# Optimization experiments

Hardware: AMD Instinct MI355X
Metric: run time of the kernel (lower is better)

The kernel has to match this reference:

```python
import jax, jax.numpy as jnp
import numpy as np

N_ITEMS = 1_000_000
N_FACTORS = 64

def setup_inputs() -> dict:
    key = jax.random.key(0)
    emb_weight = jax.random.normal(key, (N_ITEMS, N_FACTORS), dtype=jnp.float32)
    return {"emb_weight": emb_weight, "item_idx": 12345, "size": 50}

def reference(emb_weight, item_idx, size):
    # gather query row: u = emb(ind)  -> [d]
    u = emb_weight[item_idx]
    # scores = u @ emb.T  -> [n_items] (GEMV against full table)
    scores = emb_weight @ u
    # top-k retrieval (size <= n_items, clamp as in original)
    k = min(size, scores.shape[0])
    s, i = jax.lax.top_k(scores, k)
    return s, i
```

## Files before the change

### kernel.cpp

```cpp
#include <hip/hip_runtime.h>

#define NEG_INF (-1.0e30f)
#define CAP 4096
#define NBKT 4096

__device__ __forceinline__ unsigned flip(float f) {
    unsigned u = __float_as_uint(f);
    return (u & 0x80000000u) ? ~u : (u | 0x80000000u);
}

__device__ __forceinline__ bool pair_gt(float sa, int ia, float sb, int ib) {
    return (sa > sb) || (sa == sb && ia < ib);
}

__global__ __launch_bounds__(256) void k_gemv(const float* __restrict__ emb,
                                              const int* __restrict__ p_idx,
                                              float* __restrict__ scores) {
    const int tid   = threadIdx.x;
    const int col16 = tid & 15;
    const int grp   = tid >> 4;
    const float4 u4 = ((const float4*)(emb + (size_t)(*p_idx) * 64))[col16];
    const int base  = blockIdx.x * 64;
#pragma unroll
    for (int sub = 0; sub < 4; ++sub) {
        const int item = base + sub * 16 + grp;
        const float4 r = ((const float4*)(emb + (size_t)item * 64))[col16];
        float p = r.x * u4.x + r.y * u4.y + r.z * u4.z + r.w * u4.w;
        p += __shfl_xor(p, 1, 16);
        p += __shfl_xor(p, 2, 16);
        p += __shfl_xor(p, 4, 16);
        p += __shfl_xor(p, 8, 16);
        if (col16 == 0) scores[item] = p;
    }
}

__global__ __launch_bounds__(256) void k_hist(const float* __restrict__ scores,
                                              int n4, unsigned* __restrict__ hist) {
    __shared__ unsigned h[NBKT];
    const int tid = threadIdx.x;
    for (int i = tid; i < NBKT; i += 256) h[i] = 0;
    __syncthreads();
    const float4* s4 = (const float4*)scores;
    for (int i = blockIdx.x * 256 + tid; i < n4; i += gridDim.x * 256) {
        float4 v = s4[i];
        atomicAdd(&h[flip(v.x) >> 20], 1u);
        atomicAdd(&h[flip(v.y) >> 20], 1u);
        atomicAdd(&h[flip(v.z) >> 20], 1u);
        atomicAdd(&h[flip(v.w) >> 20], 1u);
    }
    __syncthreads();
    for (int i = tid; i < NBKT; i += 256) {
        unsigned c = h[i];
        if (c) atomicAdd(&hist[i], c);
    }
}

__global__ __launch_bounds__(256) void k_pick(const unsigned* __restrict__ hist,
                                              int k, unsigned* __restrict__ params) {
    __shared__ unsigned h[NBKT];
    __shared__ unsigned psum[256];
    const int tid = threadIdx.x;
    for (int i = tid; i < NBKT; i += 256) h[i] = hist[i];
    __syncthreads();
    const int base = tid * 16;
    unsigned local = 0;
#pragma unroll
    for (int j = 0; j < 16; ++j) local += h[base + j];
    psum[tid] = local;
    __syncthreads();
    for (int stride = 1; stride < 256; stride <<= 1) {
        unsigned add = (tid + stride < 256) ? psum[tid + stride] : 0u;
        __syncthreads();
        psum[tid] += add;
        __syncthreads();
    }
    unsigned c = (tid + 1 < 256) ? psum[tid + 1] : 0u;
    int found_b = -1; unsigned found_above = 0;
    for (int j = 15; j >= 0; --j) {
        unsigned hb = h[base + j];
        if (c < (unsigned)k && c + hb >= (unsigned)k) { found_b = base + j; found_above = c; }
        c += hb;
    }
    if (found_b >= 0) { params[0] = (unsigned)found_b; params[1] = found_above; }
}

__global__ __launch_bounds__(256) void k_compact(const float* __restrict__ scores,
                                                 int n4,
                                                 const unsigned* __restrict__ params,
                                                 unsigned* __restrict__ cnt,
                                                 float* __restrict__ cand_s,
                                                 int* __restrict__ cand_i) {
    const unsigned B = params[0];
    const float4* s4 = (const float4*)scores;
    for (int i = blockIdx.x * 256 + threadIdx.x; i < n4; i += gridDim.x * 256) {
        float4 v = s4[i];
        const float vv[4] = {v.x, v.y, v.z, v.w};
#pragma unroll
        for (int j = 0; j < 4; ++j) {
            if ((flip(vv[j]) >> 20) >= B) {
                unsigned pos = atomicAdd(cnt, 1u);
                if (pos < CAP) { cand_s[pos] = vv[j]; cand_i[pos] = i * 4 + j; }
            }
        }
    }
}

__global__ __launch_bounds__(256) void k_final(const float* __restrict__ cand_s,
                                               const int* __restrict__ cand_i,
                                               const unsigned* __restrict__ cnt,
                                               int k, float* __restrict__ out) {
    __shared__ float ss[CAP];
    __shared__ int   si[CAP];
    const int tid = threadIdx.x;
    unsigned c = *cnt;
    const int n = (c > CAP) ? CAP : (int)c;
    int N = 64; while (N < n) N <<= 1;
    for (int i = tid; i < N; i += 256) {
        const bool v = i < n;
        ss[i] = v ? cand_s[i] : NEG_INF;
        si[i] = v ? cand_i[i] : 0x7fffffff;
    }
    __syncthreads();
    for (int kk = 2; kk <= N; kk <<= 1) {
        for (int j = kk >> 1; j > 0; j >>= 1) {
            for (int i = tid; i < N; i += 256) {
                int l = i ^ j;
                if (l > i) {
                    float s_i = ss[i], s_l = ss[l];
                    int   d_i = si[i], d_l = si[l];
                    bool sw = ((i & kk) == 0) ? pair_gt(s_l, d_l, s_i, d_i)
                                              : pair_gt(s_i, d_i, s_l, d_l);
                    if (sw) { ss[i] = s_l; si[i] = d_l; ss[l] = s_i; si[l] = d_i; }
                }
            }
            __syncthreads();
        }
    }
    if (tid < k) {
        out[tid]     = ss[tid];
        out[k + tid] = (float)si[tid];
    }
}

extern "C" void kernel_launch(void* const* d_in, const int* in_sizes, int n_in,
                              void* d_out, int out_size, void* d_ws, size_t ws_size,
                              hipStream_t stream) {
    const float* emb   = (const float*)d_in[0];
    const int*   p_idx = (const int*)d_in[1];
    const int n_items  = in_sizes[0] / 64;
    const int k        = out_size / 2;

    float*    scores = (float*)d_ws;
    unsigned* hist   = (unsigned*)(scores + n_items);
    unsigned* params = hist + NBKT;
    unsigned* cnt    = params + 2;
    float*    cand_s = (float*)(cnt + 1);
    int*      cand_i = (int*)(cand_s + CAP);

    hipMemsetAsync(hist, 0, (NBKT + 3) * sizeof(unsigned), stream);

    const int n4 = n_items / 4;
    k_gemv   <<<n_items / 64, 256, 0, stream>>>(emb, p_idx, scores);
    k_hist   <<<128, 256, 0, stream>>>(scores, n4, hist);
    k_pick   <<<1,   256, 0, stream>>>(hist, k, params);
    k_compact<<<128, 256, 0, stream>>>(scores, n4, params, cnt, cand_s, cand_i);
    k_final  <<<1,   256, 0, stream>>>(cand_s, cand_i, cnt, k, (float*)d_out);
}
```

Before: 367.2 us.

## Fuse histogram into GEMV and merge pick, compact, and final sort kernels

The histogram build moves into the GEMV kernel, where each block covers 1024 items and updates a shared-memory histogram as scores are produced, so the separate pass that re-reads the scores disappears. The pick, compact and final-sort stages become one kernel. Every block recomputes the threshold bucket on its own, and the last block to finish, found with an atomic done counter, runs the bitonic sort. This cuts launch count from five to two and removes one full read of the scores, at the cost of redundant per-block prefix scans, larger shared memory use, and a last-block serial tail.

```diff
diff --git a/kernel.cpp b/kernel.cpp
--- a/kernel.cpp
+++ b/kernel.cpp
@@ -3,6 +3,7 @@
 #define NEG_INF (-1.0e30f)
 #define CAP 4096
 #define NBKT 4096
+#define IPB 1024
 
 __device__ __forceinline__ unsigned flip(float f) {
     unsigned u = __float_as_uint(f);
@@ -13,53 +14,61 @@
     return (sa > sb) || (sa == sb && ia < ib);
 }
 
-__global__ __launch_bounds__(256) void k_gemv(const float* __restrict__ emb,
-                                              const int* __restrict__ p_idx,
-                                              float* __restrict__ scores) {
+__global__ __launch_bounds__(256) void k_gemv_hist(const float* __restrict__ emb,
+                                                   const int* __restrict__ p_idx,
+                                                   float* __restrict__ scores,
+                                                   int n_items,
+                                                   unsigned* __restrict__ hist) {
+    __shared__ unsigned h[NBKT];
     const int tid   = threadIdx.x;
     const int col16 = tid & 15;
     const int grp   = tid >> 4;
+    for (int i = tid; i < NBKT; i += 256) h[i] = 0u;
     const float4 u4 = ((const float4*)(emb + (size_t)(*p_idx) * 64))[col16];
-    const int base  = blockIdx.x * 64;
+    const int base  = blockIdx.x * IPB;
+    __syncthreads();
+#pragma unroll 1
+    for (int c = 0; c < IPB / 64; ++c) {
+        const int cbase = base + c * 64;
+        if (cbase >= n_items) break;
 #pragma unroll
-    for (int sub = 0; sub < 4; ++sub) {
-        const int item = base + sub * 16 + grp;
-        const float4 r = ((const float4*)(emb + (size_t)item * 64))[col16];
-        float p = r.x * u4.x + r.y * u4.y + r.z * u4.z + r.w * u4.w;
-        p += __shfl_xor(p, 1, 16);
-        p += __shfl_xor(p, 2, 16);
-        p += __shfl_xor(p, 4, 16);
-        p += __shfl_xor(p, 8, 16);
-        if (col16 == 0) scores[item] = p;
+        for (int sub = 0; sub < 4; ++sub) {
+            const int item = cbase + sub * 16 + grp;
+            const float4 r = ((const float4*)(emb + (size_t)item * 64))[col16];
+            float p = r.x * u4.x + r.y * u4.y + r.z * u4.z + r.w * u4.w;
+            p += __shfl_xor(p, 1, 16);
+            p += __shfl_xor(p, 2, 16);
+            p += __shfl_xor(p, 4, 16);
+            p += __shfl_xor(p, 8, 16);
+            if (col16 == 0) {
+                scores[item] = p;
+                atomicAdd(&h[flip(p) >> 20], 1u);
+            }
+        }
+    }
+    __syncthreads();
+    for (int i = tid; i < NBKT; i += 256) {
+        unsigned cv = h[i];
+        if (cv) atomicAdd(&hist[i], cv);
     }
 }
 
-__global__ __launch_bounds__(256) void k_hist(const float* __restrict__ scores,
-                                              int n4, unsigned* __restrict__ hist) {
-    __shared__ unsigned h[NBKT];
-    const int tid = threadIdx.x;
-    for (int i = tid; i < NBKT; i += 256) h[i] = 0;
-    __syncthreads();
-    const float4* s4 = (const float4*)scores;
-    for (int i = blockIdx.x * 256 + tid; i < n4; i += gridDim.x * 256) {
-        float4 v = s4[i];
-        atomicAdd(&h[flip(v.x) >> 20], 1u);
-        atomicAdd(&h[flip(v.y) >> 20], 1u);
-        atomicAdd(&h[flip(v.z) >> 20], 1u);
-        atomicAdd(&h[flip(v.w) >> 20], 1u);
-    }
-    __syncthreads();
-    for (int i = tid; i < NBKT; i += 256) {
-        unsigned c = h[i];
-        if (c) atomicAdd(&hist[i], c);
-    }
-}
-
-__global__ __launch_bounds__(256) void k_pick(const unsigned* __restrict__ hist,
-                                              int k, unsigned* __restrict__ params) {
+__global__ __launch_bounds__(256) void k_select(const float* __restrict__ scores,
+                                                int n4, int k,
+                                                const unsigned* __restrict__ hist,
+                                                unsigned* __restrict__ cnt,
+                                                unsigned* __restrict__ done,
+                                                float* __restrict__ cand_s,
+                                                int* __restrict__ cand_i,
+                                                float* __restrict__ out) {
     __shared__ unsigned h[NBKT];
     __shared__ unsigned psum[256];
+    __shared__ unsigned sB;
+    __shared__ int s_last;
+    __shared__ float ss[CAP];
+    __shared__ int   si[CAP];
     const int tid = threadIdx.x;
+
     for (int i = tid; i < NBKT; i += 256) h[i] = hist[i];
     __syncthreads();
     const int base = tid * 16;
@@ -75,24 +84,16 @@
         __syncthreads();
     }
     unsigned c = (tid + 1 < 256) ? psum[tid + 1] : 0u;
-    int found_b = -1; unsigned found_above = 0;
     for (int j = 15; j >= 0; --j) {
         unsigned hb = h[base + j];
-        if (c < (unsigned)k && c + hb >= (unsigned)k) { found_b = base + j; found_above = c; }
+        if (c < (unsigned)k && c + hb >= (unsigned)k) sB = (unsigned)(base + j);
         c += hb;
     }
-    if (found_b >= 0) { params[0] = (unsigned)found_b; params[1] = found_above; }
-}
+    __syncthreads();
+    const unsigned B = sB;
 
-__global__ __launch_bounds__(256) void k_compact(const float* __restrict__ scores,
-                                                 int n4,
-                                                 const unsigned* __restrict__ params,
-                                                 unsigned* __restrict__ cnt,
-                                                 float* __restrict__ cand_s,
-                                                 int* __restrict__ cand_i) {
-    const unsigned B = params[0];
     const float4* s4 = (const float4*)scores;
-    for (int i = blockIdx.x * 256 + threadIdx.x; i < n4; i += gridDim.x * 256) {
+    for (int i = blockIdx.x * 256 + tid; i < n4; i += gridDim.x * 256) {
         float4 v = s4[i];
         const float vv[4] = {v.x, v.y, v.z, v.w};
 #pragma unroll
@@ -103,17 +104,18 @@
             }
         }
     }
-}
 
-__global__ __launch_bounds__(256) void k_final(const float* __restrict__ cand_s,
-                                               const int* __restrict__ cand_i,
-                                               const unsigned* __restrict__ cnt,
-                                               int k, float* __restrict__ out) {
-    __shared__ float ss[CAP];
-    __shared__ int   si[CAP];
-    const int tid = threadIdx.x;
-    unsigned c = *cnt;
-    const int n = (c > CAP) ? CAP : (int)c;
+    __threadfence();
+    if (tid == 0) {
+        unsigned t = atomicAdd(done, 1u);
+        s_last = (t == gridDim.x - 1) ? 1 : 0;
+    }
+    __syncthreads();
+    if (!s_last) return;
+    __threadfence();
+
+    unsigned cc = atomicAdd(cnt, 0u);
+    const int n = (cc > CAP) ? CAP : (int)cc;
     int N = 64; while (N < n) N <<= 1;
     for (int i = tid; i < N; i += 256) {
         const bool v = i < n;
@@ -152,17 +154,16 @@
 
     float*    scores = (float*)d_ws;
     unsigned* hist   = (unsigned*)(scores + n_items);
-    unsigned* params = hist + NBKT;
-    unsigned* cnt    = params + 2;
-    float*    cand_s = (float*)(cnt + 1);
+    unsigned* cnt    = hist + NBKT;
+    unsigned* done   = cnt + 1;
+    float*    cand_s = (float*)(done + 1);
     int*      cand_i = (int*)(cand_s + CAP);
 
-    hipMemsetAsync(hist, 0, (NBKT + 3) * sizeof(unsigned), stream);
+    hipMemsetAsync(hist, 0, (NBKT + 2) * sizeof(unsigned), stream);
 
     const int n4 = n_items / 4;
-    k_gemv   <<<n_items / 64, 256, 0, stream>>>(emb, p_idx, scores);
-    k_hist   <<<128, 256, 0, stream>>>(scores, n4, hist);
-    k_pick   <<<1,   256, 0, stream>>>(hist, k, params);
-    k_compact<<<128, 256, 0, stream>>>(scores, n4, params, cnt, cand_s, cand_i);
-    k_final  <<<1,   256, 0, stream>>>(cand_s, cand_i, cnt, k, (float*)d_out);
+    const int gb = (n_items + IPB - 1) / IPB;
+    k_gemv_hist<<<gb, 256, 0, stream>>>(emb, p_idx, scores, n_items, hist);
+    k_select   <<<256, 256, 0, stream>>>(scores, n4, k, hist, cnt, done,
+                                         cand_s, cand_i, (float*)d_out);
 }
```

New measurement: 392.5 us. 6.9% more time.

## Fuse histogram with pick and compact with final via last-block pattern

Applied to the files above, without the earlier changes.

Removes the memset by zeroing the histogram and control words inside block 0 of the GEMV kernel. The histogram and bucket-pick kernels are merged, and so are the compaction and final-sort kernels, using an atomic done counter so the last block to finish runs the serial tail. This cuts five launches plus a memset down to three launches, removing per-launch overhead and gaps between dependent kernels. In exchange it adds threadfence/atomic synchronization and larger shared memory use in the compaction kernel, which may lower its occupancy.

```diff
diff --git a/kernel.cpp b/kernel.cpp
--- a/kernel.cpp
+++ b/kernel.cpp
@@ -15,8 +15,12 @@
 
 __global__ __launch_bounds__(256) void k_gemv(const float* __restrict__ emb,
                                               const int* __restrict__ p_idx,
-                                              float* __restrict__ scores) {
+                                              float* __restrict__ scores,
+                                              unsigned* __restrict__ ctrl) {
     const int tid   = threadIdx.x;
+    if (blockIdx.x == 0) {
+        for (int i = tid; i < NBKT + 8; i += 256) ctrl[i] = 0u;
+    }
     const int col16 = tid & 15;
     const int grp   = tid >> 4;
     const float4 u4 = ((const float4*)(emb + (size_t)(*p_idx) * 64))[col16];
@@ -34,11 +38,15 @@
     }
 }
 
-__global__ __launch_bounds__(256) void k_hist(const float* __restrict__ scores,
-                                              int n4, unsigned* __restrict__ hist) {
+__global__ __launch_bounds__(256) void k_hist_pick(const float* __restrict__ scores,
+                                                   int n4, int k,
+                                                   unsigned* __restrict__ hist,
+                                                   unsigned* __restrict__ done,
+                                                   unsigned* __restrict__ params) {
     __shared__ unsigned h[NBKT];
+    __shared__ int s_last;
     const int tid = threadIdx.x;
-    for (int i = tid; i < NBKT; i += 256) h[i] = 0;
+    for (int i = tid; i < NBKT; i += 256) h[i] = 0u;
     __syncthreads();
     const float4* s4 = (const float4*)scores;
     for (int i = blockIdx.x * 256 + tid; i < n4; i += gridDim.x * 256) {
@@ -53,13 +61,14 @@
         unsigned c = h[i];
         if (c) atomicAdd(&hist[i], c);
     }
-}
 
-__global__ __launch_bounds__(256) void k_pick(const unsigned* __restrict__ hist,
-                                              int k, unsigned* __restrict__ params) {
-    __shared__ unsigned h[NBKT];
+    __threadfence();
+    if (tid == 0) s_last = (atomicAdd(done, 1u) == gridDim.x - 1) ? 1 : 0;
+    __syncthreads();
+    if (!s_last) return;
+    __threadfence();
+
     __shared__ unsigned psum[256];
-    const int tid = threadIdx.x;
     for (int i = tid; i < NBKT; i += 256) h[i] = hist[i];
     __syncthreads();
     const int base = tid * 16;
@@ -75,24 +84,28 @@
         __syncthreads();
     }
     unsigned c = (tid + 1 < 256) ? psum[tid + 1] : 0u;
-    int found_b = -1; unsigned found_above = 0;
     for (int j = 15; j >= 0; --j) {
         unsigned hb = h[base + j];
-        if (c < (unsigned)k && c + hb >= (unsigned)k) { found_b = base + j; found_above = c; }
+        if (c < (unsigned)k && c + hb >= (unsigned)k) params[0] = (unsigned)(base + j);
         c += hb;
     }
-    if (found_b >= 0) { params[0] = (unsigned)found_b; params[1] = found_above; }
 }
 
-__global__ __launch_bounds__(256) void k_compact(const float* __restrict__ scores,
-                                                 int n4,
-                                                 const unsigned* __restrict__ params,
-                                                 unsigned* __restrict__ cnt,
-                                                 float* __restrict__ cand_s,
-                                                 int* __restrict__ cand_i) {
+__global__ __launch_bounds__(256) void k_compact_final(const float* __restrict__ scores,
+                                                       int n4, int k,
+                                                       const unsigned* __restrict__ params,
+                                                       unsigned* __restrict__ cnt,
+                                                       unsigned* __restrict__ done2,
+                                                       float* __restrict__ cand_s,
+                                                       int* __restrict__ cand_i,
+                                                       float* __restrict__ out) {
+    __shared__ int s_last;
+    __shared__ float ss[CAP];
+    __shared__ int   si[CAP];
+    const int tid = threadIdx.x;
     const unsigned B = params[0];
     const float4* s4 = (const float4*)scores;
-    for (int i = blockIdx.x * 256 + threadIdx.x; i < n4; i += gridDim.x * 256) {
+    for (int i = blockIdx.x * 256 + tid; i < n4; i += gridDim.x * 256) {
         float4 v = s4[i];
         const float vv[4] = {v.x, v.y, v.z, v.w};
 #pragma unroll
@@ -103,17 +116,15 @@
             }
         }
     }
-}
 
-__global__ __launch_bounds__(256) void k_final(const float* __restrict__ cand_s,
-                                               const int* __restrict__ cand_i,
-                                               const unsigned* __restrict__ cnt,
-                                               int k, float* __restrict__ out) {
-    __shared__ float ss[CAP];
-    __shared__ int   si[CAP];
-    const int tid = threadIdx.x;
-    unsigned c = *cnt;
-    const int n = (c > CAP) ? CAP : (int)c;
+    __threadfence();
+    if (tid == 0) s_last = (atomicAdd(done2, 1u) == gridDim.x - 1) ? 1 : 0;
+    __syncthreads();
+    if (!s_last) return;
+    __threadfence();
+
+    unsigned cc = atomicAdd(cnt, 0u);
+    const int n = (cc > CAP) ? CAP : (int)cc;
     int N = 64; while (N < n) N <<= 1;
     for (int i = tid; i < N; i += 256) {
         const bool v = i < n;
@@ -154,15 +165,14 @@
     unsigned* hist   = (unsigned*)(scores + n_items);
     unsigned* params = hist + NBKT;
     unsigned* cnt    = params + 2;
-    float*    cand_s = (float*)(cnt + 1);
+    unsigned* done   = cnt + 1;
+    unsigned* done2  = done + 1;
+    float*    cand_s = (float*)(done2 + 1);
     int*      cand_i = (int*)(cand_s + CAP);
 
-    hipMemsetAsync(hist, 0, (NBKT + 3) * sizeof(unsigned), stream);
-
     const int n4 = n_items / 4;
-    k_gemv   <<<n_items / 64, 256, 0, stream>>>(emb, p_idx, scores);
-    k_hist   <<<128, 256, 0, stream>>>(scores, n4, hist);
-    k_pick   <<<1,   256, 0, stream>>>(hist, k, params);
-    k_compact<<<128, 256, 0, stream>>>(scores, n4, params, cnt, cand_s, cand_i);
-    k_final  <<<1,   256, 0, stream>>>(cand_s, cand_i, cnt, k, (float*)d_out);
+    k_gemv        <<<n_items / 64, 256, 0, stream>>>(emb, p_idx, scores, hist);
+    k_hist_pick   <<<128, 256, 0, stream>>>(scores, n4, k, hist, done, params);
+    k_compact_final<<<128, 256, 0, stream>>>(scores, n4, k, params, cnt, done2,
+                                             cand_s, cand_i, (float*)d_out);
 }
```

Result: slower. 376.4 us (+2.5%).
